# Performance work log

Measured on AMD Instinct MI355X. Metric: run time of the kernel, lower is better.

Reference implementation:

```python
import jax, jax.numpy as jnp
import numpy as np

VTH = 0.5      # sp.vth_init
TAU = 0.25     # sp.tau_mem


def setup_inputs() -> dict:
    key = jax.random.key(0)
    x = jax.random.normal(key, (64, 2048, 256), dtype=jnp.float32)  # [B, C, T]
    return {"x": x}


def reference(x):
    """LIF integrate-fire-reset over the last (time) axis.

    Per step (STBP-style lif_update):
        u_t   = tau * u_{t-1} * (1 - spike_{t-1}) + x_t   # leaky integrate + reset
        s_t   = (u_t > vth)                                # fire
    Initial u and spike are zeros (matches out[..., max(step-1,0)] at step 0).
    """
    x_t = jnp.moveaxis(x, -1, 0)  # [T, B, C] for scan over time
    u0 = jnp.zeros(x.shape[:-1], dtype=x.dtype)
    s0 = jnp.zeros(x.shape[:-1], dtype=x.dtype)

    def step(carry, xt):
        u, s_prev = carry
        u = TAU * u * (1.0 - s_prev) + xt
        s = (u > VTH).astype(x.dtype)
        return (u, s), s

    _, spikes = jax.lax.scan(step, (u0, s0), x_t)  # spikes: [T, B, C]
    return jnp.moveaxis(spikes, 0, -1)  # [B, C, T]
```

## Files before the change

### kernel.cpp

```cpp
#include <hip/hip_runtime.h>


#define T_LEN 256
#define TQ 64
#define NCH 8
#define RPB 256
#define XS_STRIDE 36

#define TAU 0.25f
#define VTH 0.5f

typedef float f32x4 __attribute__((ext_vector_type(4)));

__global__ __launch_bounds__(RPB, 2)
void lif_kernel(const float* __restrict__ x, float* __restrict__ out) {
    __shared__ __align__(16) float xs[2][RPB * XS_STRIDE];

    const int tid  = threadIdx.x;
    const int lane = tid & 63;
    const int wv   = tid >> 6;
    const long rbase = (long)blockIdx.x * RPB;

    const float4* __restrict__ x4 = reinterpret_cast<const float4*>(x);
    float* __restrict__ outp = out;

    const int qs = tid & 7;
    const int rs = tid >> 3;

    float4 p[8];
    #pragma unroll
    for (int i = 0; i < 8; ++i)
        p[i] = x4[(rbase + rs + i * 32) * TQ + qs];

    float u = 0.0f;
    bool sprev = false;

    #pragma unroll
    for (int k = 0; k < NCH; ++k) {
        float* buf = xs[k & 1];

        #pragma unroll
        for (int i = 0; i < 8; ++i)
            *reinterpret_cast<float4*>(&buf[(rs + i * 32) * XS_STRIDE + 4 * qs]) = p[i];

        asm volatile("s_waitcnt lgkmcnt(0)" ::: "memory");
        __builtin_amdgcn_s_barrier();

        if (k + 1 < NCH) {
            #pragma unroll
            for (int i = 0; i < 8; ++i)
                p[i] = x4[(rbase + rs + i * 32) * TQ + (k + 1) * 8 + qs];
        }

        float4 v[8];
        #pragma unroll
        for (int i = 0; i < 8; ++i)
            v[i] = *reinterpret_cast<const float4*>(&buf[tid * XS_STRIDE + 4 * i]);

        unsigned int m = 0;
        #pragma unroll
        for (int i = 0; i < 8; ++i) {
            float e[4] = { v[i].x, v[i].y, v[i].z, v[i].w };
            #pragma unroll
            for (int j = 0; j < 4; ++j) {
                float um = sprev ? 0.0f : __fmul_rn(TAU, u);
                u = __fadd_rn(um, e[j]);
                sprev = u > VTH;
                m |= (sprev ? 1u : 0u) << (i * 4 + j);
            }
        }

        #pragma unroll
        for (int i = 0; i < 8; ++i) {
            int rowl = i * 8 + (lane >> 3);
            unsigned int mr = (unsigned int)__shfl((int)m, rowl, 64);
            int toff = 4 * (lane & 7);
            f32x4 o;
            o[0] = ((mr >> (toff + 0)) & 1u) ? 1.0f : 0.0f;
            o[1] = ((mr >> (toff + 1)) & 1u) ? 1.0f : 0.0f;
            o[2] = ((mr >> (toff + 2)) & 1u) ? 1.0f : 0.0f;
            o[3] = ((mr >> (toff + 3)) & 1u) ? 1.0f : 0.0f;
            long gq = (rbase + wv * 64 + rowl) * (long)TQ + k * 8 + (lane & 7);
            __builtin_nontemporal_store(o, reinterpret_cast<f32x4*>(outp) + gq);
        }
    }
}

extern "C" void kernel_launch(void* const* d_in, const int* in_sizes, int n_in,
                              void* d_out, int out_size, void* d_ws, size_t ws_size,
                              hipStream_t stream) {
    const float* x = (const float*)d_in[0];
    float* out = (float*)d_out;
    const int total = in_sizes[0];
    const int nrows = total / T_LEN;
    const int blocks = nrows / RPB;
    lif_kernel<<<blocks, RPB, 0, stream>>>(x, out);
}
```

Before: 44.81 us.

## Use single-wave blocks with two-deep register prefetch, dropping block barriers

Blocks now hold a single 64-lane wavefront that owns 64 rows, so the workgroup barrier becomes a scheduling barrier only. Global loads are prefetched two chunks ahead through a double register buffer, which gives more memory-level parallelism per wave. The cost is more registers per thread and four times as many small blocks. LDS use per block is smaller, which may allow more resident blocks.

```diff
diff --git a/kernel.cpp b/kernel.cpp
--- a/kernel.cpp
+++ b/kernel.cpp
@@ -4,7 +4,7 @@
 #define T_LEN 256
 #define TQ 64
 #define NCH 8
-#define RPB 256
+#define WPB 64
 #define XS_STRIDE 36
 
 #define TAU 0.25f
@@ -12,25 +12,25 @@
 
 typedef float f32x4 __attribute__((ext_vector_type(4)));
 
-__global__ __launch_bounds__(RPB, 2)
+__global__ __launch_bounds__(WPB, 2)
 void lif_kernel(const float* __restrict__ x, float* __restrict__ out) {
-    __shared__ __align__(16) float xs[2][RPB * XS_STRIDE];
+    __shared__ __align__(16) float xs[2][WPB * XS_STRIDE];
 
-    const int tid  = threadIdx.x;
-    const int lane = tid & 63;
-    const int wv   = tid >> 6;
-    const long rbase = (long)blockIdx.x * RPB;
+    const int lane = threadIdx.x;
+    const long rbase = (long)blockIdx.x * WPB;
 
     const float4* __restrict__ x4 = reinterpret_cast<const float4*>(x);
-    float* __restrict__ outp = out;
 
-    const int qs = tid & 7;
-    const int rs = tid >> 3;
+    const int qs = lane & 7;
+    const int rs = lane >> 3;
 
-    float4 p[8];
+    float4 p[2][8];
     #pragma unroll
     for (int i = 0; i < 8; ++i)
-        p[i] = x4[(rbase + rs + i * 32) * TQ + qs];
+        p[0][i] = x4[(rbase + rs + i * 8) * TQ + 0 * 8 + qs];
+    #pragma unroll
+    for (int i = 0; i < 8; ++i)
+        p[1][i] = x4[(rbase + rs + i * 8) * TQ + 1 * 8 + qs];
 
     float u = 0.0f;
     bool sprev = false;
@@ -41,21 +41,21 @@
 
         #pragma unroll
         for (int i = 0; i < 8; ++i)
-            *reinterpret_cast<float4*>(&buf[(rs + i * 32) * XS_STRIDE + 4 * qs]) = p[i];
+            *reinterpret_cast<float4*>(&buf[(rs + i * 8) * XS_STRIDE + 4 * qs]) = p[k & 1][i];
 
         asm volatile("s_waitcnt lgkmcnt(0)" ::: "memory");
-        __builtin_amdgcn_s_barrier();
-
-        if (k + 1 < NCH) {
-            #pragma unroll
-            for (int i = 0; i < 8; ++i)
-                p[i] = x4[(rbase + rs + i * 32) * TQ + (k + 1) * 8 + qs];
-        }
+        __builtin_amdgcn_sched_barrier(0);
 
         float4 v[8];
         #pragma unroll
         for (int i = 0; i < 8; ++i)
-            v[i] = *reinterpret_cast<const float4*>(&buf[tid * XS_STRIDE + 4 * i]);
+            v[i] = *reinterpret_cast<const float4*>(&buf[lane * XS_STRIDE + 4 * i]);
+
+        if (k + 2 < NCH) {
+            #pragma unroll
+            for (int i = 0; i < 8; ++i)
+                p[k & 1][i] = x4[(rbase + rs + i * 8) * TQ + (k + 2) * 8 + qs];
+        }
 
         unsigned int m = 0;
         #pragma unroll
@@ -80,8 +80,8 @@
             o[1] = ((mr >> (toff + 1)) & 1u) ? 1.0f : 0.0f;
             o[2] = ((mr >> (toff + 2)) & 1u) ? 1.0f : 0.0f;
             o[3] = ((mr >> (toff + 3)) & 1u) ? 1.0f : 0.0f;
-            long gq = (rbase + wv * 64 + rowl) * (long)TQ + k * 8 + (lane & 7);
-            __builtin_nontemporal_store(o, reinterpret_cast<f32x4*>(outp) + gq);
+            long gq = (rbase + rowl) * (long)TQ + k * 8 + (lane & 7);
+            __builtin_nontemporal_store(o, reinterpret_cast<f32x4*>(out) + gq);
         }
     }
 }
@@ -93,6 +93,6 @@
     float* out = (float*)d_out;
     const int total = in_sizes[0];
     const int nrows = total / T_LEN;
-    const int blocks = nrows / RPB;
-    lif_kernel<<<blocks, RPB, 0, stream>>>(x, out);
+    const int blocks = nrows / WPB;
+    lif_kernel<<<blocks, WPB, 0, stream>>>(x, out);
 }
```

Measured after the change: 77.03 us. +71.9%, slower.

## Prefetch two chunks ahead with dual register sets and rolled outer loop

Applied to the files above, without the earlier changes.

Global loads now run two chunks ahead of compute, using two register prefetch sets (pA/pB) that alternate with the two LDS buffers. The outer chunk loop is rolled into four iterations of two halves each. The aim is to hide more global-load latency behind the serial LIF recurrence and to shrink code size. The cost is 32 more VGPRs for the second prefetch set, which could lower occupancy under launch_bounds(256,2). The rolled loop also adds runtime address arithmetic and a branch.

```diff
diff --git a/kernel.cpp b/kernel.cpp
--- a/kernel.cpp
+++ b/kernel.cpp
@@ -3,7 +3,6 @@
 
 #define T_LEN 256
 #define TQ 64
-#define NCH 8
 #define RPB 256
 #define XS_STRIDE 36
 
@@ -22,68 +21,70 @@
     const long rbase = (long)blockIdx.x * RPB;
 
     const float4* __restrict__ x4 = reinterpret_cast<const float4*>(x);
-    float* __restrict__ outp = out;
 
     const int qs = tid & 7;
     const int rs = tid >> 3;
 
-    float4 p[8];
-    #pragma unroll
+    float4 pA[8], pB[8];
+    #pragma unroll 8
     for (int i = 0; i < 8; ++i)
-        p[i] = x4[(rbase + rs + i * 32) * TQ + qs];
+        pA[i] = x4[(rbase + rs + i * 32) * TQ + 0 * 8 + qs];
+    #pragma unroll 8
+    for (int i = 0; i < 8; ++i)
+        pB[i] = x4[(rbase + rs + i * 32) * TQ + 1 * 8 + qs];
 
     float u = 0.0f;
     bool sprev = false;
 
-    #pragma unroll
-    for (int k = 0; k < NCH; ++k) {
-        float* buf = xs[k & 1];
+#define HALF(P, BUF, KC, KP)                                                     \
+    {                                                                            \
+        _Pragma("unroll 8")                                                      \
+        for (int i = 0; i < 8; ++i)                                              \
+            *reinterpret_cast<float4*>(&BUF[(rs + i * 32) * XS_STRIDE + 4 * qs]) = P[i]; \
+        asm volatile("s_waitcnt lgkmcnt(0)" ::: "memory");                       \
+        __builtin_amdgcn_s_barrier();                                            \
+        if ((KP) < 8) {                                                          \
+            _Pragma("unroll 8")                                                  \
+            for (int i = 0; i < 8; ++i)                                          \
+                P[i] = x4[(rbase + rs + i * 32) * TQ + (KP) * 8 + qs];           \
+        }                                                                        \
+        float4 v[8];                                                             \
+        _Pragma("unroll 8")                                                      \
+        for (int i = 0; i < 8; ++i)                                              \
+            v[i] = *reinterpret_cast<const float4*>(&BUF[tid * XS_STRIDE + 4 * i]); \
+        unsigned int m = 0;                                                      \
+        _Pragma("unroll 8")                                                      \
+        for (int i = 0; i < 8; ++i) {                                            \
+            float e[4] = { v[i].x, v[i].y, v[i].z, v[i].w };                     \
+            _Pragma("unroll 4")                                                  \
+            for (int j = 0; j < 4; ++j) {                                        \
+                float um = sprev ? 0.0f : __fmul_rn(TAU, u);                     \
+                u = __fadd_rn(um, e[j]);                                         \
+                sprev = u > VTH;                                                 \
+                m |= (sprev ? 1u : 0u) << (i * 4 + j);                           \
+            }                                                                    \
+        }                                                                        \
+        _Pragma("unroll 8")                                                      \
+        for (int i = 0; i < 8; ++i) {                                            \
+            int rowl = i * 8 + (lane >> 3);                                      \
+            unsigned int mr = (unsigned int)__shfl((int)m, rowl, 64);            \
+            int toff = 4 * (lane & 7);                                           \
+            f32x4 o;                                                             \
+            o[0] = ((mr >> (toff + 0)) & 1u) ? 1.0f : 0.0f;                      \
+            o[1] = ((mr >> (toff + 1)) & 1u) ? 1.0f : 0.0f;                      \
+            o[2] = ((mr >> (toff + 2)) & 1u) ? 1.0f : 0.0f;                      \
+            o[3] = ((mr >> (toff + 3)) & 1u) ? 1.0f : 0.0f;                      \
+            long gq = (rbase + wv * 64 + rowl) * (long)TQ + (KC) * 8 + (lane & 7); \
+            __builtin_nontemporal_store(o, reinterpret_cast<f32x4*>(out) + gq);  \
+        }                                                                        \
+    }
 
-        #pragma unroll
-        for (int i = 0; i < 8; ++i)
-            *reinterpret_cast<float4*>(&buf[(rs + i * 32) * XS_STRIDE + 4 * qs]) = p[i];
-
-        asm volatile("s_waitcnt lgkmcnt(0)" ::: "memory");
-        __builtin_amdgcn_s_barrier();
-
-        if (k + 1 < NCH) {
-            #pragma unroll
-            for (int i = 0; i < 8; ++i)
-                p[i] = x4[(rbase + rs + i * 32) * TQ + (k + 1) * 8 + qs];
-        }
-
-        float4 v[8];
-        #pragma unroll
-        for (int i = 0; i < 8; ++i)
-            v[i] = *reinterpret_cast<const float4*>(&buf[tid * XS_STRIDE + 4 * i]);
-
-        unsigned int m = 0;
-        #pragma unroll
-        for (int i = 0; i < 8; ++i) {
-            float e[4] = { v[i].x, v[i].y, v[i].z, v[i].w };
-            #pragma unroll
-            for (int j = 0; j < 4; ++j) {
-                float um = sprev ? 0.0f : __fmul_rn(TAU, u);
-                u = __fadd_rn(um, e[j]);
-                sprev = u > VTH;
-                m |= (sprev ? 1u : 0u) << (i * 4 + j);
-            }
-        }
-
-        #pragma unroll
-        for (int i = 0; i < 8; ++i) {
-            int rowl = i * 8 + (lane >> 3);
-            unsigned int mr = (unsigned int)__shfl((int)m, rowl, 64);
-            int toff = 4 * (lane & 7);
-            f32x4 o;
-            o[0] = ((mr >> (toff + 0)) & 1u) ? 1.0f : 0.0f;
-            o[1] = ((mr >> (toff + 1)) & 1u) ? 1.0f : 0.0f;
-            o[2] = ((mr >> (toff + 2)) & 1u) ? 1.0f : 0.0f;
-            o[3] = ((mr >> (toff + 3)) & 1u) ? 1.0f : 0.0f;
-            long gq = (rbase + wv * 64 + rowl) * (long)TQ + k * 8 + (lane & 7);
-            __builtin_nontemporal_store(o, reinterpret_cast<f32x4*>(outp) + gq);
-        }
+    for (int kk = 0; kk < 4; ++kk) {
+        const int k0 = 2 * kk;
+        HALF(pA, (xs[0]), k0, k0 + 2)
+        HALF(pB, (xs[1]), k0 + 1, k0 + 3)
     }
+#undef HALF
 }
 
 extern "C" void kernel_launch(void* const* d_in, const int* in_sizes, int n_in,
```

New measurement: 81.09 us. 1.81x slower.
